# Kernel tuning notes

Measured on AMD Instinct MI355X. Metric: run time of the kernel, lower is better.

The kernel has to match this reference:

```python
import jax, jax.numpy as jnp
import numpy as np

N_HEAD = 16
N_EMBD = 1024
BLOCK = 2048
B, T = 4, 2048


def setup_inputs() -> dict:
    key = jax.random.key(0)
    ks = jax.random.split(key, 5)
    scale = 1.0 / np.sqrt(N_EMBD)
    return {
        "x": jax.random.normal(ks[0], (B, T, N_EMBD), dtype=jnp.float32),
        "W_attn": jax.random.normal(ks[1], (N_EMBD, 3 * N_EMBD), dtype=jnp.float32) * scale,
        "b_attn": jax.random.normal(ks[2], (3 * N_EMBD,), dtype=jnp.float32) * 0.02,
        "W_proj": jax.random.normal(ks[3], (N_EMBD, N_EMBD), dtype=jnp.float32) * scale,
        "b_proj": jax.random.normal(ks[4], (N_EMBD,), dtype=jnp.float32) * 0.02,
    }


def reference(x, W_attn, b_attn, W_proj, b_proj):
    Bb, Tt, C = x.shape
    hd = C // N_HEAD
    qkv = x @ W_attn + b_attn                      # [B,T,3C]
    q, k, v = jnp.split(qkv, 3, axis=2)
    # [B,H,T,hd]
    q = q.reshape(Bb, Tt, N_HEAD, hd).transpose(0, 2, 1, 3)
    k = k.reshape(Bb, Tt, N_HEAD, hd).transpose(0, 2, 1, 3)
    v = v.reshape(Bb, Tt, N_HEAD, hd).transpose(0, 2, 1, 3)
    att = jnp.einsum('bhqd,bhkd->bhqk', q, k) / np.sqrt(hd).astype(x.dtype)
    causal = jnp.tril(jnp.ones((Tt, Tt), dtype=bool))
    att = jnp.where(causal[None, None], att, jnp.finfo(att.dtype).min)
    att = jax.nn.softmax(att, axis=-1)
    y = jnp.einsum('bhqk,bhkd->bhqd', att, v)      # [B,H,T,hd]
    y = y.transpose(0, 2, 1, 3).reshape(Bb, Tt, C)
    return y @ W_proj + b_proj
```

## Files before the change

kernel.cpp:

```cpp
#include <hip/hip_runtime.h>
#include <stdint.h>

typedef unsigned short u16;
typedef __bf16 bf16;
typedef bf16 bf16x8 __attribute__((ext_vector_type(8)));
typedef float f32x4 __attribute__((ext_vector_type(4)));
typedef u16 u16x8 __attribute__((ext_vector_type(8)));
typedef u16 u16x4 __attribute__((ext_vector_type(4)));

#define T_SEQ 2048
#define NHEAD 16
#define HD    64
#define CEMB  1024
#define QS    8388608
#define QSCALE 0.18033688011112042f

#define BARRIER() asm volatile("s_barrier" ::: "memory")
#define WAITV(N)  asm volatile("s_waitcnt vmcnt(" #N ")" ::: "memory")

__device__ __forceinline__ u16 f2b(float f){
  bf16 h = (bf16)f;
  return __builtin_bit_cast(u16, h);
}
__device__ __forceinline__ void glds16(const void* g, const void* l){
  __builtin_amdgcn_global_load_lds(
    (__attribute__((address_space(1))) unsigned int*)(uintptr_t)g,
    (__attribute__((address_space(3))) unsigned int*)(uintptr_t)l,
    16, 0, 0);
}

__global__ __launch_bounds__(256) void prep_kernel(
    const float* __restrict__ x, u16* __restrict__ xb,
    const float* __restrict__ Wa, u16* __restrict__ Wta,
    const float* __restrict__ Wp, u16* __restrict__ Wtp)
{
  __shared__ __align__(16) u16 tile[64][72];
  const int bid = blockIdx.x;
  const int tid = threadIdx.x;
  if (bid < 4096){
    const int i = (bid * 256 + tid) * 8;
    f32x4 a = *(const f32x4*)&x[i];
    f32x4 b = *(const f32x4*)&x[i + 4];
    u16x8 h;
    #pragma unroll
    for (int j = 0; j < 4; j++){ h[j] = f2b(a[j]); h[4+j] = f2b(b[j]); }
    *(u16x8*)&xb[i] = h;
    return;
  }
  const float* src; u16* dst; int K, N, bx, by;
  if (bid < 4864){ const int j = bid - 4096; src = Wa; dst = Wta; K = 1024; N = 3072; bx = j % 48; by = j / 48; }
  else           { const int j = bid - 4864; src = Wp; dst = Wtp; K = 1024; N = 1024; bx = j % 16; by = j / 16; }
  const int n0 = bx * 64, k0 = by * 64;
  #pragma unroll
  for (int it = 0; it < 4; it++){
    const int idx = it * 256 + tid;
    const int row = idx >> 4, c4 = (idx & 15) * 4;
    f32x4 v = *(const f32x4*)&src[(size_t)(k0 + row) * N + n0 + c4];
    #pragma unroll
    for (int j = 0; j < 4; j++) tile[row][c4 + j] = f2b(v[j]);
  }
  __syncthreads();
  const int r = tid >> 3, cc = (tid & 7) * 8;
  #pragma unroll
  for (int i = 0; i < 2; i++){
    const int rr = r + i * 32;
    u16x8 v;
    #pragma unroll
    for (int j = 0; j < 8; j++) v[j] = tile[cc + j][rr];
    *(u16x8*)&dst[(size_t)(n0 + rr) * K + k0 + cc] = v;
  }
}

#define QSTAGE(BUF, K0) do{ \
  _Pragma("unroll") \
  for (int ii = 0; ii < 4; ii++){ \
    const int slot0 = (wave*4 + ii) * 64; \
    const int s = slot0 + lane; \
    const int row = s >> 3; \
    const int cc8 = ((s & 7) ^ (row & 7)) * 8; \
    glds16(&A [(size_t)(m0 + row) * Ktot + (K0) + cc8], &As[BUF][slot0*8]); \
    glds16(&Bt[(size_t)(n0 + row) * Ktot + (K0) + cc8], &Bs[BUF][slot0*8]); \
  } \
}while(0)

__global__ __launch_bounds__(256) void gemm_qkv128(
    const u16* __restrict__ A, const u16* __restrict__ Bt,
    const float* __restrict__ bias, u16* __restrict__ out, int Ktot)
{
  __shared__ __align__(16) u16 As[2][128*64];
  __shared__ __align__(16) u16 Bs[2][128*64];
  const int tid = threadIdx.x;
  const int lane = tid & 63, wave = tid >> 6;
  const int l15 = lane & 15, l4 = lane >> 4;
  const int wm = wave >> 1, wn = wave & 1;
  const int id = blockIdx.x;
  const int m0 = (id / 24) * 128, n0 = (id % 24) * 128;
  const int NT = Ktot >> 6;

  f32x4 acc[4][4] = {};

  QSTAGE(0, 0);
  for (int c = 0; c < NT; c++){
    const int cur = c & 1;
    if (c + 1 < NT){
      QSTAGE(cur ^ 1, (c + 1) * 64);
      WAITV(8);
    } else {
      WAITV(0);
    }
    BARRIER();

    #pragma unroll
    for (int ks = 0; ks < 2; ks++){
      bf16x8 af[4], bfr[4];
      #pragma unroll
      for (int mt = 0; mt < 4; mt++){
        const int rf = wm*64 + mt*16 + l15;
        const int slot = rf*8 + ((ks*4 + l4) ^ (rf & 7));
        af[mt] = *(const bf16x8*)&As[cur][slot*8];
      }
      #pragma unroll
      for (int nt = 0; nt < 4; nt++){
        const int rf = wn*64 + nt*16 + l15;
        const int slot = rf*8 + ((ks*4 + l4) ^ (rf & 7));
        bfr[nt] = *(const bf16x8*)&Bs[cur][slot*8];
      }
      #pragma unroll
      for (int mt = 0; mt < 4; mt++)
        #pragma unroll
        for (int nt = 0; nt < 4; nt++)
          acc[mt][nt] = __builtin_amdgcn_mfma_f32_16x16x32_bf16(
              af[mt], bfr[nt], acc[mt][nt], 0, 0, 0);
    }
    BARRIER();
  }

  #pragma unroll
  for (int nt = 0; nt < 4; nt++){
    const int n = n0 + wn*64 + nt*16 + l15;
    const float bias_v = bias[n];
    const int which = n >> 10;
    const int cc = n & 1023;
    const int h = cc >> 6, d = cc & 63;
    const float sc = (which == 0) ? QSCALE : 1.0f;
    if (which == 2){
      #pragma unroll
      for (int mt = 0; mt < 4; mt++){
        const int rowg = m0 + wm*64 + mt*16 + l4*4;
        const int bb = rowg >> 11, t = rowg & 2047;
        u16x4 pk;
        #pragma unroll
        for (int r = 0; r < 4; r++) pk[r] = f2b(acc[mt][nt][r] + bias_v);
        *(u16x4*)&out[(size_t)2*QS + ((size_t)(bb*NHEAD + h)*HD + d)*T_SEQ + t] = pk;
      }
    } else {
      #pragma unroll
      for (int mt = 0; mt < 4; mt++)
        #pragma unroll
        for (int r = 0; r < 4; r++){
          const int rowg = m0 + wm*64 + mt*16 + l4*4 + r;
          const int bb = rowg >> 11, t = rowg & 2047;
          out[(size_t)which*QS + ((size_t)(bb*NHEAD + h)*T_SEQ + t)*HD + d]
              = f2b((acc[mt][nt][r] + bias_v) * sc);
        }
    }
  }
}

__global__ __launch_bounds__(256) void gemm_proj(
    const u16* __restrict__ A, const u16* __restrict__ Bt,
    const float* __restrict__ bias, float* __restrict__ out, int Ktot)
{
  __shared__ __align__(16) u16 As[2][128*64];
  __shared__ __align__(16) u16 Bs[2][128*64];
  const int tid = threadIdx.x;
  const int lane = tid & 63, wave = tid >> 6;
  const int l15 = lane & 15, l4 = lane >> 4;
  const int wm = wave >> 1, wn = wave & 1;
  const int id = blockIdx.x;
  const int swz = (id & 7) * 64 + (id >> 3);
  const int m0 = (swz / 8) * 128, n0 = (swz % 8) * 128;
  const int NT = Ktot >> 6;

  f32x4 acc[4][4] = {};

  QSTAGE(0, 0);
  for (int c = 0; c < NT; c++){
    const int cur = c & 1;
    if (c + 1 < NT){
      QSTAGE(cur ^ 1, (c + 1) * 64);
      WAITV(8);
    } else {
      WAITV(0);
    }
    BARRIER();

    #pragma unroll
    for (int ks = 0; ks < 2; ks++){
      bf16x8 af[4], bfr[4];
      #pragma unroll
      for (int mt = 0; mt < 4; mt++){
        const int rf = wm*64 + mt*16 + l15;
        const int slot = rf*8 + ((ks*4 + l4) ^ (rf & 7));
        af[mt] = *(const bf16x8*)&As[cur][slot*8];
      }
      #pragma unroll
      for (int nt = 0; nt < 4; nt++){
        const int rf = wn*64 + nt*16 + l15;
        const int slot = rf*8 + ((ks*4 + l4) ^ (rf & 7));
        bfr[nt] = *(const bf16x8*)&Bs[cur][slot*8];
      }
      #pragma unroll
      for (int mt = 0; mt < 4; mt++)
        #pragma unroll
        for (int nt = 0; nt < 4; nt++)
          acc[mt][nt] = __builtin_amdgcn_mfma_f32_16x16x32_bf16(
              af[mt], bfr[nt], acc[mt][nt], 0, 0, 0);
    }
    BARRIER();
  }

  #pragma unroll
  for (int nt = 0; nt < 4; nt++){
    const int n = n0 + wn*64 + nt*16 + l15;
    const float bias_v = bias[n];
    #pragma unroll
    for (int mt = 0; mt < 4; mt++)
      #pragma unroll
      for (int r = 0; r < 4; r++){
        const int rowg = m0 + wm*64 + mt*16 + l4*4 + r;
        out[(size_t)rowg*CEMB + n] = acc[mt][nt][r] + bias_v;
      }
  }
}

__global__ __launch_bounds__(256, 3) void attn_kernel(
    const u16* __restrict__ qb, const u16* __restrict__ kb,
    const u16* __restrict__ vtb, u16* __restrict__ y)
{
  __shared__ __align__(16) u16 Ks[2*64*64];
  __shared__ __align__(16) u16 Vt[2*64*64];
  __shared__ __align__(16) u16 Pw[8*16*72];
  const int tid = threadIdx.x;
  const int lane = tid & 63, wave = tid >> 6;
  const int l15 = lane & 15, l4 = lane >> 4;
  const int qt = 15 - (blockIdx.x >> 6);
  const int bh = blockIdx.x & 63;
  const int q0 = qt * 128;
  const size_t base = (size_t)bh * (T_SEQ * HD);
  const u16* qp  = qb  + base;
  const u16* kp  = kb  + base;
  const u16* vtp = vtb + base;

  const int qmin0 = q0 + wave*32;
  const int qmin1 = qmin0 + 16;

  bf16x8 qf[2][2];
  #pragma unroll
  for (int g = 0; g < 2; g++){
    const int m = qmin0 + g*16 + l15;
    qf[g][0] = *(const bf16x8*)&qp[m*HD +      l4*8];
    qf[g][1] = *(const bf16x8*)&qp[m*HD + 32 + l4*8];
  }
  f32x4 o[2][4] = {};
  float l_run[2] = {0.f, 0.f};

  const int s0i = (wave*2 + 0) * 64 + lane;
  const int s1i = (wave*2 + 1) * 64 + lane;
  const int row0 = s0i >> 3, c0 = (s0i & 7) ^ (row0 & 7);
  const int row1 = s1i >> 3, c1 = (s1i & 7) ^ (row1 & 7);
  const int koff0 = row0*HD + c0*8, koff1 = row1*HD + c1*8;
  const int voff0 = row0*T_SEQ + c0*8, voff1 = row1*T_SEQ + c1*8;
  const int ldso0 = (wave*2 + 0) * 64 * 8, ldso1 = (wave*2 + 1) * 64 * 8;

  const int nkt = 2*qt + 2;

  glds16(&kp [koff0], &Ks[ldso0]);
  glds16(&kp [koff1], &Ks[ldso1]);
  glds16(&vtp[voff0], &Vt[ldso0]);
  glds16(&vtp[voff1], &Vt[ldso1]);

  for (int kt = 0; kt < nkt; kt++){
    const int cb = (kt & 1) * 4096;
    if (kt + 1 < nkt){
      const int nb = ((kt + 1) & 1) * 4096;
      glds16(&kp [(kt+1)*4096 + koff0], &Ks[nb + ldso0]);
      glds16(&kp [(kt+1)*4096 + koff1], &Ks[nb + ldso1]);
      glds16(&vtp[(kt+1)*64   + voff0], &Vt[nb + ldso0]);
      glds16(&vtp[(kt+1)*64   + voff1], &Vt[nb + ldso1]);
      WAITV(4);
    } else {
      WAITV(0);
    }
    BARRIER();

    const int t0 = kt*64;
    if (t0 <= qmin1 + 15){
      const bool act0 = (t0 <= qmin0 + 15);

      f32x4 s0[4], s1[4];
      #pragma unroll
      for (int nb2 = 0; nb2 < 4; nb2++){
        f32x4 a0 = {}, a1 = {};
        #pragma unroll
        for (int ks = 0; ks < 2; ks++){
          const int rf = nb2*16 + l15;
          const int slot = rf*8 + ((ks*4 + l4) ^ (rf & 7));
          bf16x8 kf = *(const bf16x8*)&Ks[cb + slot*8];
          a1 = __builtin_amdgcn_mfma_f32_16x16x32_bf16(kf, qf[1][ks], a1, 0, 0, 0);
          if (act0)
            a0 = __builtin_amdgcn_mfma_f32_16x16x32_bf16(kf, qf[0][ks], a0, 0, 0, 0);
        }
        s1[nb2] = a1; s0[nb2] = a0;
      }

      #pragma unroll
      for (int g = 0; g < 2; g++){
        if (g == 0 && !act0) continue;
        f32x4* sf = (g == 0) ? s0 : s1;
        const int qmin = (g == 0) ? qmin0 : qmin1;
        const int qg = qmin + l15;
        float lsum = 0.f;
        if (t0 + 63 > qmin){
          #pragma unroll
          for (int nb2 = 0; nb2 < 4; nb2++){
            u16x4 pk;
            #pragma unroll
            for (int r = 0; r < 4; r++){
              const int t = t0 + nb2*16 + l4*4 + r;
              float p = __builtin_amdgcn_exp2f(sf[nb2][r]);
              p = (t <= qg) ? p : 0.0f;
              lsum += p;
              pk[r] = f2b(p);
            }
            *(u16x4*)&Pw[(wave*2 + g)*1152 + l15*72 + nb2*16 + l4*4] = pk;
          }
        } else {
          #pragma unroll
          for (int nb2 = 0; nb2 < 4; nb2++){
            u16x4 pk;
            #pragma unroll
            for (int r = 0; r < 4; r++){
              const float p = __builtin_amdgcn_exp2f(sf[nb2][r]);
              lsum += p;
              pk[r] = f2b(p);
            }
            *(u16x4*)&Pw[(wave*2 + g)*1152 + l15*72 + nb2*16 + l4*4] = pk;
          }
        }
        l_run[g] += lsum;
      }

      #pragma unroll
      for (int ks = 0; ks < 2; ks++){
        bf16x8 pf1 = *(const bf16x8*)&Pw[(wave*2 + 1)*1152 + l15*72 + ks*32 + l4*8];
        bf16x8 pf0;
        if (act0) pf0 = *(const bf16x8*)&Pw[(wave*2 + 0)*1152 + l15*72 + ks*32 + l4*8];
        #pragma unroll
        for (int nh = 0; nh < 4; nh++){
          const int rf = nh*16 + l15;
          const int slot = rf*8 + ((ks*4 + l4) ^ (rf & 7));
          bf16x8 vf = *(const bf16x8*)&Vt[cb + slot*8];
          o[1][nh] = __builtin_amdgcn_mfma_f32_16x16x32_bf16(vf, pf1, o[1][nh], 0, 0, 0);
          if (act0)
            o[0][nh] = __builtin_amdgcn_mfma_f32_16x16x32_bf16(vf, pf0, o[0][nh], 0, 0, 0);
        }
      }
    }
    BARRIER();
  }

  const int b = bh >> 4, h = bh & 15;
  #pragma unroll
  for (int g = 0; g < 2; g++){
    float lr = l_run[g];
    lr += __shfl_xor(lr, 16);
    lr += __shfl_xor(lr, 32);
    const float inv_l = 1.0f / lr;
    const int t = qmin0 + g*16 + l15;
    #pragma unroll
    for (int nh = 0; nh < 4; nh++){
      u16x4 pk;
      #pragma unroll
      for (int r = 0; r < 4; r++) pk[r] = f2b(o[g][nh][r] * inv_l);
      *(u16x4*)&y[((size_t)(b*T_SEQ + t))*CEMB + h*HD + nh*16 + l4*4] = pk;
    }
  }
}

extern "C" void kernel_launch(void* const* d_in, const int* in_sizes, int n_in,
                              void* d_out, int out_size, void* d_ws, size_t ws_size,
                              hipStream_t stream) {
  const float* x      = (const float*)d_in[0];
  const float* W_attn = (const float*)d_in[1];
  const float* b_attn = (const float*)d_in[2];
  const float* W_proj = (const float*)d_in[3];
  const float* b_proj = (const float*)d_in[4];
  float* out = (float*)d_out;
  u16* ws  = (u16*)d_ws;

  u16* Wt_attn = ws;
  u16* Wt_proj = ws + 3145728;
  u16* xb      = ws + 4194304;
  u16* qkv     = ws + 12582912;
  u16* y       = xb;

  prep_kernel<<<5120, 256, 0, stream>>>(x, xb, W_attn, Wt_attn, W_proj, Wt_proj);
  gemm_qkv128<<<1536, 256, 0, stream>>>(xb, Wt_attn, b_attn, qkv, 1024);
  attn_kernel<<<1024, 256, 0, stream>>>(qkv, qkv + QS, qkv + 2*QS, y);
  gemm_proj<<<512, 256, 0, stream>>>(y, Wt_proj, b_proj, out, 1024);
}
```

Baseline: 227.1 us.

## Shrink QKV GEMM K-tile to 32 for occupancy and XOR-swizzle attention P buffer

Replaces the 128x128x64 QKV GEMM with a K=32 variant. It halves shared memory per block to 32KB, uses a two-rows-per-line swizzled layout with precomputed LDS offsets, and requests four blocks per CU so more blocks run concurrently and hide latency. Separately, the attention kernel's P staging buffer drops its padded 72-element stride for an XOR-swizzled 64-element stride, cutting LDS use while avoiding bank conflicts. The GEMM trade-off is twice as many K iterations, each with its own pair of barriers.

```diff
diff --git a/kernel.cpp b/kernel.cpp
--- a/kernel.cpp
+++ b/kernel.cpp
@@ -71,6 +71,104 @@
   }
 }
 
+#define QSTAGE32(BUF, K0) do{ \
+  glds16(&A [(size_t)(m0 + ga0) * Ktot + (K0) + gk0], &As[BUF][(size_t)tid*8]); \
+  glds16(&A [(size_t)(m0 + ga1) * Ktot + (K0) + gk1], &As[BUF][(size_t)(tid+256)*8]); \
+  glds16(&Bt[(size_t)(n0 + ga0) * Ktot + (K0) + gk0], &Bs[BUF][(size_t)tid*8]); \
+  glds16(&Bt[(size_t)(n0 + ga1) * Ktot + (K0) + gk1], &Bs[BUF][(size_t)(tid+256)*8]); \
+}while(0)
+
+__global__ __launch_bounds__(256, 4) void gemm_qkv32(
+    const u16* __restrict__ A, const u16* __restrict__ Bt,
+    const float* __restrict__ bias, u16* __restrict__ out, int Ktot)
+{
+  __shared__ __align__(16) u16 As[2][4096];
+  __shared__ __align__(16) u16 Bs[2][4096];
+  const int tid = threadIdx.x;
+  const int lane = tid & 63, wave = tid >> 6;
+  const int l15 = lane & 15, l4 = lane >> 4;
+  const int wm = wave >> 1, wn = wave & 1;
+  const int id = blockIdx.x;
+  const int m0 = (id / 24) * 128, n0 = (id % 24) * 128;
+  const int NT = Ktot >> 5;
+
+  int ga0, gk0, ga1, gk1;
+  { const int p = tid;       const int L = p >> 3, s = (p & 7) ^ (L & 7);
+    ga0 = 2*L + (s >> 2); gk0 = (s & 3) * 8; }
+  { const int p = tid + 256; const int L = p >> 3, s = (p & 7) ^ (L & 7);
+    ga1 = 2*L + (s >> 2); gk1 = (s & 3) * 8; }
+
+  int aoff[4], boff[4];
+  #pragma unroll
+  for (int f = 0; f < 4; f++){
+    { const int rf = wm*64 + f*16 + l15;
+      const int L = rf >> 1, phys = (((rf & 1) << 2) + l4) ^ (L & 7);
+      aoff[f] = L*64 + phys*8; }
+    { const int rf = wn*64 + f*16 + l15;
+      const int L = rf >> 1, phys = (((rf & 1) << 2) + l4) ^ (L & 7);
+      boff[f] = L*64 + phys*8; }
+  }
+
+  f32x4 acc[4][4] = {};
+
+  QSTAGE32(0, 0);
+  for (int c = 0; c < NT; c++){
+    const int cur = c & 1;
+    if (c + 1 < NT){
+      QSTAGE32(cur ^ 1, (c + 1) * 32);
+      WAITV(4);
+    } else {
+      WAITV(0);
+    }
+    BARRIER();
+
+    bf16x8 af[4], bfr[4];
+    #pragma unroll
+    for (int mt = 0; mt < 4; mt++) af[mt]  = *(const bf16x8*)&As[cur][aoff[mt]];
+    #pragma unroll
+    for (int nt = 0; nt < 4; nt++) bfr[nt] = *(const bf16x8*)&Bs[cur][boff[nt]];
+    #pragma unroll
+    for (int mt = 0; mt < 4; mt++)
+      #pragma unroll
+      for (int nt = 0; nt < 4; nt++)
+        acc[mt][nt] = __builtin_amdgcn_mfma_f32_16x16x32_bf16(
+            af[mt], bfr[nt], acc[mt][nt], 0, 0, 0);
+
+    BARRIER();
+  }
+
+  #pragma unroll
+  for (int nt = 0; nt < 4; nt++){
+    const int n = n0 + wn*64 + nt*16 + l15;
+    const float bias_v = bias[n];
+    const int which = n >> 10;
+    const int cc = n & 1023;
+    const int h = cc >> 6, d = cc & 63;
+    const float sc = (which == 0) ? QSCALE : 1.0f;
+    if (which == 2){
+      #pragma unroll
+      for (int mt = 0; mt < 4; mt++){
+        const int rowg = m0 + wm*64 + mt*16 + l4*4;
+        const int bb = rowg >> 11, t = rowg & 2047;
+        u16x4 pk;
+        #pragma unroll
+        for (int r = 0; r < 4; r++) pk[r] = f2b(acc[mt][nt][r] + bias_v);
+        *(u16x4*)&out[(size_t)2*QS + ((size_t)(bb*NHEAD + h)*HD + d)*T_SEQ + t] = pk;
+      }
+    } else {
+      #pragma unroll
+      for (int mt = 0; mt < 4; mt++)
+        #pragma unroll
+        for (int r = 0; r < 4; r++){
+          const int rowg = m0 + wm*64 + mt*16 + l4*4 + r;
+          const int bb = rowg >> 11, t = rowg & 2047;
+          out[(size_t)which*QS + ((size_t)(bb*NHEAD + h)*T_SEQ + t)*HD + d]
+              = f2b((acc[mt][nt][r] + bias_v) * sc);
+        }
+    }
+  }
+}
+
 #define QSTAGE(BUF, K0) do{ \
   _Pragma("unroll") \
   for (int ii = 0; ii < 4; ii++){ \
@@ -82,90 +180,6 @@
     glds16(&Bt[(size_t)(n0 + row) * Ktot + (K0) + cc8], &Bs[BUF][slot0*8]); \
   } \
 }while(0)
-
-__global__ __launch_bounds__(256) void gemm_qkv128(
-    const u16* __restrict__ A, const u16* __restrict__ Bt,
-    const float* __restrict__ bias, u16* __restrict__ out, int Ktot)
-{
-  __shared__ __align__(16) u16 As[2][128*64];
-  __shared__ __align__(16) u16 Bs[2][128*64];
-  const int tid = threadIdx.x;
-  const int lane = tid & 63, wave = tid >> 6;
-  const int l15 = lane & 15, l4 = lane >> 4;
-  const int wm = wave >> 1, wn = wave & 1;
-  const int id = blockIdx.x;
-  const int m0 = (id / 24) * 128, n0 = (id % 24) * 128;
-  const int NT = Ktot >> 6;
-
-  f32x4 acc[4][4] = {};
-
-  QSTAGE(0, 0);
-  for (int c = 0; c < NT; c++){
-    const int cur = c & 1;
-    if (c + 1 < NT){
-      QSTAGE(cur ^ 1, (c + 1) * 64);
-      WAITV(8);
-    } else {
-      WAITV(0);
-    }
-    BARRIER();
-
-    #pragma unroll
-    for (int ks = 0; ks < 2; ks++){
-      bf16x8 af[4], bfr[4];
-      #pragma unroll
-      for (int mt = 0; mt < 4; mt++){
-        const int rf = wm*64 + mt*16 + l15;
-        const int slot = rf*8 + ((ks*4 + l4) ^ (rf & 7));
-        af[mt] = *(const bf16x8*)&As[cur][slot*8];
-      }
-      #pragma unroll
-      for (int nt = 0; nt < 4; nt++){
-        const int rf = wn*64 + nt*16 + l15;
-        const int slot = rf*8 + ((ks*4 + l4) ^ (rf & 7));
-        bfr[nt] = *(const bf16x8*)&Bs[cur][slot*8];
-      }
-      #pragma unroll
-      for (int mt = 0; mt < 4; mt++)
-        #pragma unroll
-        for (int nt = 0; nt < 4; nt++)
-          acc[mt][nt] = __builtin_amdgcn_mfma_f32_16x16x32_bf16(
-              af[mt], bfr[nt], acc[mt][nt], 0, 0, 0);
-    }
-    BARRIER();
-  }
-
-  #pragma unroll
-  for (int nt = 0; nt < 4; nt++){
-    const int n = n0 + wn*64 + nt*16 + l15;
-    const float bias_v = bias[n];
-    const int which = n >> 10;
-    const int cc = n & 1023;
-    const int h = cc >> 6, d = cc & 63;
-    const float sc = (which == 0) ? QSCALE : 1.0f;
-    if (which == 2){
-      #pragma unroll
-      for (int mt = 0; mt < 4; mt++){
-        const int rowg = m0 + wm*64 + mt*16 + l4*4;
-        const int bb = rowg >> 11, t = rowg & 2047;
-        u16x4 pk;
-        #pragma unroll
-        for (int r = 0; r < 4; r++) pk[r] = f2b(acc[mt][nt][r] + bias_v);
-        *(u16x4*)&out[(size_t)2*QS + ((size_t)(bb*NHEAD + h)*HD + d)*T_SEQ + t] = pk;
-      }
-    } else {
-      #pragma unroll
-      for (int mt = 0; mt < 4; mt++)
-        #pragma unroll
-        for (int r = 0; r < 4; r++){
-          const int rowg = m0 + wm*64 + mt*16 + l4*4 + r;
-          const int bb = rowg >> 11, t = rowg & 2047;
-          out[(size_t)which*QS + ((size_t)(bb*NHEAD + h)*T_SEQ + t)*HD + d]
-              = f2b((acc[mt][nt][r] + bias_v) * sc);
-        }
-    }
-  }
-}
 
 __global__ __launch_bounds__(256) void gemm_proj(
     const u16* __restrict__ A, const u16* __restrict__ Bt,
@@ -240,7 +254,7 @@
 {
   __shared__ __align__(16) u16 Ks[2*64*64];
   __shared__ __align__(16) u16 Vt[2*64*64];
-  __shared__ __align__(16) u16 Pw[8*16*72];
+  __shared__ __align__(16) u16 Pw[8*16*64];
   const int tid = threadIdx.x;
   const int lane = tid & 63, wave = tid >> 6;
   const int l15 = lane & 15, l4 = lane >> 4;
@@ -272,6 +286,10 @@
   const int koff0 = row0*HD + c0*8, koff1 = row1*HD + c1*8;
   const int voff0 = row0*T_SEQ + c0*8, voff1 = row1*T_SEQ + c1*8;
   const int ldso0 = (wave*2 + 0) * 64 * 8, ldso1 = (wave*2 + 1) * 64 * 8;
+
+  const int px7 = l15 & 7;
+  const int pwb0 = (wave*2 + 0) * 1024 + l15*64;
+  const int pwb1 = (wave*2 + 1) * 1024 + l15*64;
 
   const int nkt = 2*qt + 2;
 
@@ -318,6 +336,7 @@
       for (int g = 0; g < 2; g++){
         if (g == 0 && !act0) continue;
         f32x4* sf = (g == 0) ? s0 : s1;
+        const int pwb = (g == 0) ? pwb0 : pwb1;
         const int qmin = (g == 0) ? qmin0 : qmin1;
         const int qg = qmin + l15;
         float lsum = 0.f;
@@ -333,7 +352,8 @@
               lsum += p;
               pk[r] = f2b(p);
             }
-            *(u16x4*)&Pw[(wave*2 + g)*1152 + l15*72 + nb2*16 + l4*4] = pk;
+            const int ps = (nb2*2 + (l4 >> 1)) ^ px7;
+            *(u16x4*)&Pw[pwb + ps*8 + (l4 & 1)*4] = pk;
           }
         } else {
           #pragma unroll
@@ -345,7 +365,8 @@
               lsum += p;
               pk[r] = f2b(p);
             }
-            *(u16x4*)&Pw[(wave*2 + g)*1152 + l15*72 + nb2*16 + l4*4] = pk;
+            const int ps = (nb2*2 + (l4 >> 1)) ^ px7;
+            *(u16x4*)&Pw[pwb + ps*8 + (l4 & 1)*4] = pk;
           }
         }
         l_run[g] += lsum;
@@ -353,9 +374,10 @@
 
       #pragma unroll
       for (int ks = 0; ks < 2; ks++){
-        bf16x8 pf1 = *(const bf16x8*)&Pw[(wave*2 + 1)*1152 + l15*72 + ks*32 + l4*8];
+        const int prs = (ks*4 + l4) ^ px7;
+        bf16x8 pf1 = *(const bf16x8*)&Pw[pwb1 + prs*8];
         bf16x8 pf0;
-        if (act0) pf0 = *(const bf16x8*)&Pw[(wave*2 + 0)*1152 + l15*72 + ks*32 + l4*8];
+        if (act0) pf0 = *(const bf16x8*)&Pw[pwb0 + prs*8];
         #pragma unroll
         for (int nh = 0; nh < 4; nh++){
           const int rf = nh*16 + l15;
@@ -406,7 +428,7 @@
   u16* y       = xb;
 
   prep_kernel<<<5120, 256, 0, stream>>>(x, xb, W_attn, Wt_attn, W_proj, Wt_proj);
-  gemm_qkv128<<<1536, 256, 0, stream>>>(xb, Wt_attn, b_attn, qkv, 1024);
+  gemm_qkv32<<<1536, 256, 0, stream>>>(xb, Wt_attn, b_attn, qkv, 1024);
   attn_kernel<<<1024, 256, 0, stream>>>(qkv, qkv + QS, qkv + 2*QS, y);
   gemm_proj<<<512, 256, 0, stream>>>(y, Wt_proj, b_proj, out, 1024);
 }
```

Result: no change. 228.2 us (+0.5%).
